# Kernel optimization log

Hardware: AMD Instinct MI355X
Metric: run time of the kernel (lower is better)

Reference implementation:

```python
import jax, jax.numpy as jnp
import numpy as np

B, S, D, H = 8, 2048, 1024, 16
HD = D // H  # head_dim = 64


def setup_inputs() -> dict:
    key = jax.random.key(0)
    ks = jax.random.split(key, 10)
    s = 0.02
    return {
        "x": jax.random.normal(ks[0], (B, S, D), jnp.float32),
        "mask": jnp.zeros((B, 1, S), jnp.float32),
        "Wq": jax.random.normal(ks[1], (D, D), jnp.float32) * s,
        "bq": jnp.zeros((D,), jnp.float32),
        "Wk": jax.random.normal(ks[2], (D, D), jnp.float32) * s,
        "bk": jnp.zeros((D,), jnp.float32),
        "Wv": jax.random.normal(ks[3], (D, D), jnp.float32) * s,
        "bv": jnp.zeros((D,), jnp.float32),
        "wa": jax.random.normal(ks[4], (HD, 1), jnp.float32) * s,
        "ba": jnp.zeros((1,), jnp.float32),
        "wb": jax.random.normal(ks[5], (HD, 1), jnp.float32) * s,
        "bb": jnp.zeros((1,), jnp.float32),
        "Wu": jax.random.normal(ks[6], (HD, HD), jnp.float32) * s,
        "bu": jnp.zeros((HD,), jnp.float32),
        "Wo": jax.random.normal(ks[7], (D, D), jnp.float32) * s,
        "bo": jnp.zeros((D,), jnp.float32),
        "gamma": jnp.ones((D,), jnp.float32),
        "beta_ln": jnp.zeros((D,), jnp.float32),
    }


def _split_heads(t):
    # [B,S,D] -> [B,H,S,HD]
    return t.reshape(B, S, H, HD).transpose(0, 2, 1, 3)


def reference(x, mask, Wq, bq, Wk, bk, Wv, bv, wa, ba, wb, bb, Wu, bu, Wo, bo, gamma, beta_ln):
    scale = 1.0 / jnp.sqrt(jnp.float32(HD))
    q = _split_heads(x @ Wq + bq)  # [B,H,S,HD]
    k = _split_heads(x @ Wk + bk)
    v = _split_heads(x @ Wv + bv)

    # additive attention over queries -> global query vector per head
    alphascore = (jnp.squeeze(q @ wa, -1) + ba[0]) * scale + mask  # [B,H,S]
    alphaw = jax.nn.softmax(alphascore, axis=-1)
    q_av = jnp.einsum('bhs,bhsd->bhd', alphaw, q)

    p = k * q_av[:, :, None, :]  # gated keys [B,H,S,HD]
    betascore = (jnp.squeeze(p @ wb, -1) + bb[0]) * scale + mask
    betaw = jax.nn.softmax(betascore, axis=-1)
    p_av = jnp.einsum('bhs,bhsd->bhd', betaw, p)

    u = v * p_av[:, :, None, :]  # gated values
    r = u @ Wu + bu  # [B,H,S,HD]
    newr = (r + q).transpose(0, 2, 1, 3).reshape(B, S, D)
    attn_out = newr @ Wo + bo

    h = x + attn_out
    mu = jnp.mean(h, axis=-1, keepdims=True)
    var = jnp.mean(jnp.square(h - mu), axis=-1, keepdims=True)
    return (h - mu) * jax.lax.rsqrt(var + 1e-6) * gamma + beta_ln
```

## Files before the change

### kernel.cpp

```cpp
#include <hip/hip_runtime.h>
#include <cstdint>

#define BB 8
#define SS 2048
#define DD 1024
#define HH 16
#define HDIM 64
#define MTOT (BB*SS)
#define QKVW 2048

typedef __attribute__((ext_vector_type(8))) __bf16 bf16x8;
typedef __attribute__((ext_vector_type(4))) float f32x4;

#define AS1(p) ((const __attribute__((address_space(1))) void*)(p))
#define AS3(p) ((__attribute__((address_space(3))) void*)(p))

__device__ __forceinline__ float bf2f(uint16_t u){
  return __uint_as_float(((uint32_t)u) << 16);
}
__device__ __forceinline__ uint16_t f2bf(float f){
  uint32_t u = __float_as_uint(f);
  return (uint16_t)((u + 0x7fffu + ((u >> 16) & 1u)) >> 16);
}

__global__ __launch_bounds__(256)
void k_prep(const float* __restrict__ x,
            const float* __restrict__ Wq, const float* __restrict__ Wk,
            const float* __restrict__ Wv, const float* __restrict__ Wo,
            const float* __restrict__ bq, const float* __restrict__ bv,
            uint16_t* __restrict__ xb, uint16_t* __restrict__ Wt,
            uint16_t* __restrict__ Wkt, uint16_t* __restrict__ WoT,
            float* __restrict__ bqv)
{
  __shared__ float t[32][33];
  const int blk = blockIdx.x, tid = threadIdx.x;
  if (blk < 2048){
    const int n4 = MTOT*DD/4;
    for (int i = blk*256 + tid; i < n4; i += 2048*256){
      float4 v = reinterpret_cast<const float4*>(x)[i];
      ushort4 o;
      o.x = f2bf(v.x); o.y = f2bf(v.y); o.z = f2bf(v.z); o.w = f2bf(v.w);
      reinterpret_cast<ushort4*>(xb)[i] = o;
    }
  } else if (blk < 6144){
    const int zb = blk - 2048;
    const int z = zb >> 10, rem = zb & 1023;
    const int by = rem >> 5, bx = rem & 31;
    const float* src = (z==0)?Wq:(z==1)?Wv:(z==2)?Wk:Wo;
    uint16_t* dst = (z==0)?Wt:(z==1)?(Wt + 1024*1024):(z==2)?Wkt:WoT;
    const int k0 = by*32, n0 = bx*32;
    const int tx = tid & 31, ty = tid >> 5;
    #pragma unroll
    for (int r = 0; r < 4; ++r)
      t[ty + r*8][tx] = src[(size_t)(k0 + ty + r*8)*1024 + n0 + tx];
    __syncthreads();
    #pragma unroll
    for (int r = 0; r < 4; ++r)
      dst[(size_t)(n0 + ty + r*8)*1024 + k0 + tx] = f2bf(t[tx][ty + r*8]);
  } else {
    const int i = (blk - 6144)*256 + tid;
    if (i < QKVW)
      bqv[i] = (i < 1024) ? bq[i] : bv[i-1024];
  }
}

#define BARRIER __builtin_amdgcn_s_barrier()

#define READA(BUF, MH) { \
  const uint16_t* _sl = lds + ((BUF)*4 + (MH))*8192; \
  _Pragma("unroll") \
  for (int f = 0; f < 4; ++f) \
    _Pragma("unroll") \
    for (int ks = 0; ks < 2; ++ks) \
      a[f][ks] = *(const bf16x8*)(_sl + (wm*64 + f*16 + l15)*64 + (((ks*4 + l4) ^ l7)<<3)); \
}

#define READB(BUF, NH, BV) { \
  const uint16_t* _sl = lds + ((BUF)*4 + 2 + (NH))*8192; \
  _Pragma("unroll") \
  for (int j = 0; j < 2; ++j) \
    _Pragma("unroll") \
    for (int ks = 0; ks < 2; ++ks) \
      BV[j][ks] = *(const bf16x8*)(_sl + (wn*32 + j*16 + l15)*64 + (((ks*4 + l4) ^ l7)<<3)); \
}

#define MMA(MH, NH, BV) { \
  __builtin_amdgcn_s_setprio(1); \
  _Pragma("unroll") \
  for (int ks = 0; ks < 2; ++ks) \
    _Pragma("unroll") \
    for (int f = 0; f < 4; ++f) \
      _Pragma("unroll") \
      for (int j = 0; j < 2; ++j) \
        acc[(MH)*4+f][(NH)*2+j] = __builtin_amdgcn_mfma_f32_16x16x32_bf16(a[f][ks], BV[j][ks], acc[(MH)*4+f][(NH)*2+j], 0, 0, 0); \
  __builtin_amdgcn_s_setprio(0); }

#define STAGEA(T, H) { \
  char* _d = (char*)lds + ((((T)&1)*4 + (H))*16384) + wave*1024; \
  _Pragma("unroll") \
  for (int l = 0; l < 2; ++l) \
    __builtin_amdgcn_global_load_lds(AS1(pA + (l*131072 + (H)*65536 + (T)*64)), AS3(_d + l*8192), 16, 0, 0); \
}

#define STAGEB(T, H) { \
  char* _d = (char*)lds + ((((T)&1)*4 + 2 + (H))*16384) + wave*1024; \
  _Pragma("unroll") \
  for (int l = 0; l < 2; ++l) \
    __builtin_amdgcn_global_load_lds(AS1(pB + (l*131072 + (H)*32768 + (T)*64)), AS3(_d + l*8192), 16, 0, 0); \
}

template<int EPI, int NB_T>
__global__ __launch_bounds__(512)
void k_gemm256(const uint16_t* __restrict__ A, const uint16_t* __restrict__ Bt,
               const float* __restrict__ bias, const uint16_t* __restrict__ resid16,
               uint16_t* __restrict__ Cout,
               const float* __restrict__ waP, const float* __restrict__ baP,
               const float* __restrict__ maskP,
               float* __restrict__ cpartA, float* __restrict__ dpartA)
{
  constexpr int N = NB_T * 256;
  __shared__ uint16_t lds[8 * 8192];
  const int tid = threadIdx.x;
  const int lane = tid & 63, wave = tid >> 6;
  const int wm = wave >> 2, wn = wave & 3;
  const int l15 = lane & 15, l4 = lane >> 4, l7 = lane & 7;

  const int nwg = gridDim.x, cpx = nwg >> 3, bid = blockIdx.x;
  const int wg = (bid & 7) * cpx + (bid >> 3);
  const int m0 = (wg / NB_T) << 8, n0 = (wg % NB_T) << 8;

  const int colbase = (((tid & 7) ^ ((tid >> 3) & 7)) << 3);
  const uint16_t* pA = A  + (size_t)(m0 + (tid >> 3)) * 1024 + colbase;
  const uint16_t* pB = Bt + (size_t)(n0 + ((tid >> 8) << 6) + ((tid >> 3) & 31)) * 1024 + colbase;

  f32x4 acc[8][4] = {};
  bf16x8 a[4][2], b0[2][2], b1[2][2];

  STAGEA(0,0); STAGEB(0,1); STAGEA(0,1); STAGEB(0,0);
  STAGEA(1,0); STAGEB(1,1); STAGEA(1,1);
  asm volatile("s_waitcnt vmcnt(6)" ::: "memory");
  BARRIER;

  #pragma unroll
  for (int I = 0; I < 7; ++I){
    const int e = 2*I;
    READA(0,0); READB(0,0,b0); STAGEB(e+1, 0);
    BARRIER; MMA(0,0,b0); BARRIER;
    READB(0,1,b1); STAGEA(e+2, 0);
    BARRIER; MMA(0,1,b1); BARRIER;
    READA(0,1); STAGEB(e+2, 1);
    BARRIER; MMA(1,1,b1); BARRIER;
    STAGEA(e+2, 1);
    asm volatile("s_waitcnt vmcnt(6)" ::: "memory");
    BARRIER; MMA(1,0,b0); BARRIER;
    READA(1,0); READB(1,0,b0); STAGEB(e+2, 0);
    BARRIER; MMA(0,0,b0); BARRIER;
    READB(1,1,b1); STAGEA(e+3, 0);
    BARRIER; MMA(0,1,b1); BARRIER;
    READA(1,1); STAGEB(e+3, 1);
    BARRIER; MMA(1,1,b1); BARRIER;
    STAGEA(e+3, 1);
    asm volatile("s_waitcnt vmcnt(6)" ::: "memory");
    BARRIER; MMA(1,0,b0); BARRIER;
  }

  {
    READA(0,0); READB(0,0,b0); STAGEB(15, 0);
    BARRIER; MMA(0,0,b0); BARRIER;
    READB(0,1,b1);
    BARRIER; MMA(0,1,b1); BARRIER;
    READA(0,1);
    BARRIER; MMA(1,1,b1); BARRIER;
    asm volatile("s_waitcnt vmcnt(0)" ::: "memory");
    BARRIER; MMA(1,0,b0); BARRIER;
    READA(1,0); READB(1,0,b0);
    BARRIER; MMA(0,0,b0); BARRIER;
    READB(1,1,b1);
    BARRIER; MMA(0,1,b1); BARRIER;
    READA(1,1);
    BARRIER; MMA(1,1,b1); BARRIER;
    MMA(1,0,b0);
  }

  #pragma unroll
  for (int mh = 0; mh < 2; ++mh)
  #pragma unroll
  for (int f = 0; f < 4; ++f)
  #pragma unroll
  for (int nh = 0; nh < 2; ++nh)
  #pragma unroll
  for (int j = 0; j < 2; ++j){
    const int gcol = n0 + wn*64 + nh*32 + j*16 + l15;
    const float bi = bias[gcol];
    const int rbase = m0 + wm*128 + mh*64 + f*16 + l4*4;
    #pragma unroll
    for (int rr = 0; rr < 4; ++rr){
      const size_t idx = (size_t)(rbase + rr)*N + gcol;
      float v = acc[mh*4+f][nh*2+j][rr] + bi;
      if (EPI == 1) v += bf2f(resid16[idx]);
      Cout[idx] = f2bf(v);
    }
  }

  if (EPI == 0 && n0 < 1024){
    const int hg = (n0 >> 6) + wn;
    const float bav = baP[0];
    float bcol[2][2], wv[2][2];
    #pragma unroll
    for (int nh = 0; nh < 2; ++nh)
    #pragma unroll
    for (int j = 0; j < 2; ++j){
      const int c = nh*32 + j*16 + l15;
      bcol[nh][j] = bias[n0 + wn*64 + c];
      wv[nh][j]   = waP[c];
    }
    float colacc[2][2] = {{0.f,0.f},{0.f,0.f}};
    float esum = 0.f;
    #pragma unroll
    for (int mh = 0; mh < 2; ++mh)
    #pragma unroll
    for (int f = 0; f < 4; ++f)
    #pragma unroll
    for (int rr = 0; rr < 4; ++rr){
      float qv[2][2];
      float p = 0.f;
      #pragma unroll
      for (int nh = 0; nh < 2; ++nh)
      #pragma unroll
      for (int j = 0; j < 2; ++j){
        qv[nh][j] = acc[mh*4+f][nh*2+j][rr] + bcol[nh][j];
        p += qv[nh][j] * wv[nh][j];
      }
      p += __shfl_xor(p, 1); p += __shfl_xor(p, 2);
      p += __shfl_xor(p, 4); p += __shfl_xor(p, 8);
      const int grow = m0 + wm*128 + mh*64 + f*16 + l4*4 + rr;
      const float E = __expf((p + bav)*0.125f + maskP[grow]);
      esum += E;
      #pragma unroll
      for (int nh = 0; nh < 2; ++nh)
      #pragma unroll
      for (int j = 0; j < 2; ++j)
        colacc[nh][j] += E * qv[nh][j];
    }
    const int rb = (m0 >> 7) + wm;
    #pragma unroll
    for (int nh = 0; nh < 2; ++nh)
    #pragma unroll
    for (int j = 0; j < 2; ++j){
      float v = colacc[nh][j];
      v += __shfl_xor(v, 16); v += __shfl_xor(v, 32);
      if (l4 == 0)
        cpartA[(size_t)rb*1024 + n0 + wn*64 + nh*32 + j*16 + l15] = v;
    }
    esum += __shfl_xor(esum, 16); esum += __shfl_xor(esum, 32);
    if (lane == 0) dpartA[rb*16 + hg] = esum;
  }
}

__global__ __launch_bounds__(256)
void k_mergeA(const float* __restrict__ cpartA, const float* __restrict__ dpartA,
              const float* __restrict__ wb,
              float* __restrict__ qavB, float* __restrict__ wvecB)
{
  __shared__ float dsum[16];
  const int blk = blockIdx.x, tid = threadIdx.x;
  const int b = blk >> 2, c = (blk & 3)*256 + tid;
  if (tid < 16){
    float d = 0.f;
    #pragma unroll
    for (int rb = 0; rb < 16; ++rb) d += dpartA[(b*16 + rb)*16 + tid];
    dsum[tid] = d;
  }
  __syncthreads();
  float s = 0.f;
  #pragma unroll
  for (int rb = 0; rb < 16; ++rb) s += cpartA[(size_t)(b*16 + rb)*1024 + c];
  const float qv = s / dsum[(c >> 6) & 15];
  qavB[b*1024 + c]  = qv;
  wvecB[b*1024 + c] = qv * wb[c & 63];
}

__global__ __launch_bounds__(256)
void k_foldB(const uint16_t* __restrict__ Wkt, const float* __restrict__ wvecB,
             const float* __restrict__ bk, const float* __restrict__ bbP,
             float* __restrict__ pBg, float* __restrict__ csB)
{
  __shared__ float wl[64];
  __shared__ float redc[64];
  const int bh = blockIdx.x, b = bh >> 4, h = bh & 15;
  const int tid = threadIdx.x;
  if (tid < 64) wl[tid] = wvecB[b*1024 + h*64 + tid];
  __syncthreads();
  const int k0 = tid*4;
  float a0 = 0.f, a1 = 0.f, a2 = 0.f, a3 = 0.f;
  for (int d = 0; d < 64; ++d){
    const float w = wl[d];
    const ushort4 r = *(const ushort4*)(Wkt + (size_t)(h*64 + d)*1024 + k0);
    a0 += bf2f(r.x)*w; a1 += bf2f(r.y)*w; a2 += bf2f(r.z)*w; a3 += bf2f(r.w)*w;
  }
  float* dst = pBg + (size_t)bh*1024 + k0;
  dst[0] = a0; dst[1] = a1; dst[2] = a2; dst[3] = a3;
  if (tid < 64) redc[tid] = bk[h*64 + tid] * wl[tid];
  __syncthreads();
  if (tid == 0){
    float s = 0.f;
    for (int i = 0; i < 64; ++i) s += redc[i];
    csB[bh] = s + bbP[0];
  }
}

__global__ __launch_bounds__(512)
void k_poolX(const uint16_t* __restrict__ xb, const float* __restrict__ pBg,
             const float* __restrict__ csB, const float* __restrict__ mask,
             float* __restrict__ xwp, float* __restrict__ dpartB)
{
  const int blk = blockIdx.x, tid = threadIdx.x;
  const int b = blk >> 5;
  const int h = tid >> 5, cs = tid & 31;
  const int col0 = cs*32;

  float pr[32];
  {
    const float4* p4 = (const float4*)(pBg + (size_t)(b*16 + h)*1024 + col0);
    #pragma unroll
    for (int i = 0; i < 8; ++i){
      const float4 t = p4[i];
      pr[4*i] = t.x; pr[4*i+1] = t.y; pr[4*i+2] = t.z; pr[4*i+3] = t.w;
    }
  }
  const float csh = csB[b*16 + h];
  float acc[32];
  #pragma unroll
  for (int i = 0; i < 32; ++i) acc[i] = 0.f;
  float esum = 0.f;

  const int row0 = blk*64;
  for (int r = 0; r < 64; ++r){
    const int row = row0 + r;
    const uint16_t* xr = xb + (size_t)row*1024 + col0;
    float xv[32];
    #pragma unroll
    for (int i = 0; i < 4; ++i){
      const bf16x8 v = *(const bf16x8*)(xr + i*8);
      #pragma unroll
      for (int e = 0; e < 8; ++e) xv[i*8+e] = (float)v[e];
    }
    float s = 0.f;
    #pragma unroll
    for (int i = 0; i < 32; ++i) s += xv[i]*pr[i];
    s += __shfl_xor(s, 1); s += __shfl_xor(s, 2); s += __shfl_xor(s, 4);
    s += __shfl_xor(s, 8); s += __shfl_xor(s, 16);
    const float E = __expf((s + csh)*0.125f + mask[row]);
    esum += E;
    #pragma unroll
    for (int i = 0; i < 32; ++i) acc[i] += E*xv[i];
  }
  float* dst = xwp + (size_t)(blk*16 + h)*1024 + col0;
  #pragma unroll
  for (int i = 0; i < 8; ++i)
    ((float4*)dst)[i] = (float4){acc[4*i], acc[4*i+1], acc[4*i+2], acc[4*i+3]};
  if (cs == 0) dpartB[blk*16 + h] = esum;
}

__global__ __launch_bounds__(512)
void k_finalB(const float* __restrict__ xwp, const float* __restrict__ dpartB,
              const float* __restrict__ qavB, const uint16_t* __restrict__ Wkt,
              const float* __restrict__ bk, const float* __restrict__ Wu,
              uint16_t* __restrict__ WuPT)
{
  __shared__ float xwl[1024];
  __shared__ float kvl[64];
  __shared__ float pavl[64];
  __shared__ float dsh;
  const int bh = blockIdx.x, b = bh >> 4, h = bh & 15;
  const int tid = threadIdx.x;
  #pragma unroll
  for (int i = 0; i < 2; ++i){
    const int idx = i*512 + tid;
    float s = 0.f;
    #pragma unroll
    for (int rc = 0; rc < 32; ++rc)
      s += xwp[((size_t)(b*32 + rc)*16 + h)*1024 + idx];
    xwl[idx] = s;
  }
  if (tid < 32){
    float d = dpartB[(b*32 + tid)*16 + h];
    d += __shfl_xor(d, 1); d += __shfl_xor(d, 2); d += __shfl_xor(d, 4);
    d += __shfl_xor(d, 8); d += __shfl_xor(d, 16);
    if (tid == 0) dsh = d;
  }
  __syncthreads();
  const int d = tid >> 3, q = tid & 7;
  const uint16_t* wrow = Wkt + (size_t)(h*64 + d)*1024 + q*128;
  const float* xwq = xwl + q*128;
  float s = 0.f;
  #pragma unroll
  for (int i = 0; i < 16; ++i){
    const bf16x8 v = *(const bf16x8*)(wrow + i*8);
    #pragma unroll
    for (int e = 0; e < 8; ++e) s += (float)v[e]*xwq[i*8+e];
  }
  s += __shfl_xor(s, 1); s += __shfl_xor(s, 2); s += __shfl_xor(s, 4);
  if (q == 0) kvl[d] = s;
  __syncthreads();
  if (tid < 64)
    pavl[tid] = qavB[b*1024 + h*64 + tid] * (kvl[tid]/dsh + bk[h*64 + tid]);
  __syncthreads();
  uint16_t* dst = WuPT + (size_t)bh*4096;
  for (int idx = tid; idx < 4096; idx += 512){
    const int i = idx & 63, jcol = idx >> 6;
    dst[idx] = f2bf(pavl[i]*Wu[i*64 + jcol]);
  }
}

__global__ __launch_bounds__(256)
void k_newr(const uint16_t* __restrict__ qkv, const uint16_t* __restrict__ WuPT,
            const float* __restrict__ bu, uint16_t* __restrict__ newr)
{
  const int bh = blockIdx.x >> 3, st = blockIdx.x & 7;
  const int b = bh >> 4, h = bh & 15;
  const int tid = threadIdx.x, wave = tid >> 6, lane = tid & 63;
  const int l15 = lane & 15, l4 = lane >> 4;
  const int s0 = st*256 + wave*64;
  const uint16_t* vb = qkv + 1024 + h*64;
  const uint16_t* wt = WuPT + (size_t)bh*4096;

  f32x4 acc[4][4] = {};
  #pragma unroll
  for (int ks = 0; ks < 2; ++ks){
    bf16x8 bfr[4];
    #pragma unroll
    for (int n = 0; n < 4; ++n)
      bfr[n] = *(const bf16x8*)(wt + (n*16 + l15)*64 + ks*32 + l4*8);
    #pragma unroll
    for (int m = 0; m < 4; ++m){
      const int s = s0 + m*16 + l15;
      bf16x8 af = *(const bf16x8*)(vb + (size_t)(b*SS + s)*QKVW + ks*32 + l4*8);
      #pragma unroll
      for (int n = 0; n < 4; ++n)
        acc[m][n] = __builtin_amdgcn_mfma_f32_16x16x32_bf16(af, bfr[n], acc[m][n], 0, 0, 0);
    }
  }
  #pragma unroll
  for (int n = 0; n < 4; ++n){
    const int j = n*16 + l15;
    const float bj = bu[j];
    #pragma unroll
    for (int m = 0; m < 4; ++m){
      #pragma unroll
      for (int r = 0; r < 4; ++r){
        const int s = s0 + m*16 + l4*4 + r;
        const size_t qidx = (size_t)(b*SS + s)*QKVW + h*64 + j;
        const float q = bf2f(qkv[qidx]);
        newr[(size_t)(b*SS + s)*DD + h*64 + j] = f2bf(acc[m][n][r] + bj + q);
      }
    }
  }
}

__global__ __launch_bounds__(256)
void k_ln(const uint16_t* __restrict__ h16, const float* __restrict__ gamma,
          const float* __restrict__ beta, float* __restrict__ out)
{
  __shared__ float r1[256], r2[256];
  const int row = blockIdx.x, tid = threadIdx.x;
  const ushort4 hv = ((const ushort4*)(h16 + (size_t)row*DD))[tid];
  float v0 = bf2f(hv.x), v1 = bf2f(hv.y), v2 = bf2f(hv.z), v3 = bf2f(hv.w);
  float s  = v0 + v1 + v2 + v3;
  float ss = v0*v0 + v1*v1 + v2*v2 + v3*v3;
  r1[tid] = s; r2[tid] = ss; __syncthreads();
  for (int off = 128; off > 0; off >>= 1){
    if (tid < off){ r1[tid] += r1[tid+off]; r2[tid] += r2[tid+off]; }
    __syncthreads();
  }
  const float mu  = r1[0]*(1.f/1024.f);
  const float var = r2[0]*(1.f/1024.f) - mu*mu;
  const float inv = rsqrtf(var + 1e-6f);
  const float4 g  = ((const float4*)gamma)[tid];
  const float4 be = ((const float4*)beta)[tid];
  float4 o;
  o.x = (v0-mu)*inv*g.x + be.x;
  o.y = (v1-mu)*inv*g.y + be.y;
  o.z = (v2-mu)*inv*g.z + be.z;
  o.w = (v3-mu)*inv*g.w + be.w;
  ((float4*)(out + (size_t)row*DD))[tid] = o;
}

extern "C" void kernel_launch(void* const* d_in, const int* in_sizes, int n_in,
                              void* d_out, int out_size, void* d_ws, size_t ws_size,
                              hipStream_t stream) {
  const float* x    = (const float*)d_in[0];
  const float* mask = (const float*)d_in[1];
  const float* Wq   = (const float*)d_in[2];
  const float* bq   = (const float*)d_in[3];
  const float* Wk   = (const float*)d_in[4];
  const float* bk   = (const float*)d_in[5];
  const float* Wv   = (const float*)d_in[6];
  const float* bv   = (const float*)d_in[7];
  const float* wa   = (const float*)d_in[8];
  const float* ba   = (const float*)d_in[9];
  const float* wb   = (const float*)d_in[10];
  const float* bb   = (const float*)d_in[11];
  const float* Wu   = (const float*)d_in[12];
  const float* bu   = (const float*)d_in[13];
  const float* Wo   = (const float*)d_in[14];
  const float* bo   = (const float*)d_in[15];
  const float* gamma= (const float*)d_in[16];
  const float* beta = (const float*)d_in[17];
  float* out = (float*)d_out;

  char* ws = (char*)d_ws;
  const size_t MB = 1ull << 20;
  uint16_t* xb    = (uint16_t*)(ws);
  uint16_t* Wt    = (uint16_t*)(ws + 32*MB);
  uint16_t* Wkt   = (uint16_t*)(ws + 36*MB);
  uint16_t* WoT   = (uint16_t*)(ws + 38*MB);
  float*    bqv   = (float*)   (ws + 40*MB);
  uint16_t* WuPT  = (uint16_t*)(ws + 41*MB);
  uint16_t* qkv   = (uint16_t*)(ws + 42*MB);
  uint16_t* hbuf16= (uint16_t*)(ws + 42*MB);
  float* cpartA = (float*)(ws + 110*MB);
  float* dpartA = (float*)(ws + 111*MB);
  float* qavB   = (float*)(ws + 112*MB);
  float* wvecB  = (float*)(ws + 113*MB);
  float* pBg    = (float*)(ws + 114*MB);
  float* csB    = (float*)(ws + 115*MB);
  float* dpartB = (float*)(ws + 116*MB);
  float* xwp    = (float*)(ws + 117*MB);
  uint16_t* newr= (uint16_t*)(ws + 138*MB);

  k_prep<<<6156, 256, 0, stream>>>(x, Wq, Wk, Wv, Wo, bq, bv, xb, Wt, Wkt, WoT, bqv);

  k_gemm256<0,8><<<(MTOT/256)*(QKVW/256), 512, 0, stream>>>(
      xb, Wt, bqv, nullptr, qkv, wa, ba, mask, cpartA, dpartA);

  k_mergeA<<<32, 256, 0, stream>>>(cpartA, dpartA, wb, qavB, wvecB);
  k_foldB<<<128, 256, 0, stream>>>(Wkt, wvecB, bk, bb, pBg, csB);
  k_poolX<<<256, 512, 0, stream>>>(xb, pBg, csB, mask, xwp, dpartB);
  k_finalB<<<128, 512, 0, stream>>>(xwp, dpartB, qavB, Wkt, bk, Wu, WuPT);

  k_newr<<<BB*HH*8, 256, 0, stream>>>(qkv, WuPT, bu, newr);
  k_gemm256<1,4><<<(MTOT/256)*(DD/256), 512, 0, stream>>>(
      newr, WoT, bo, xb, hbuf16, nullptr, nullptr, nullptr, nullptr, nullptr);
  k_ln<<<MTOT, 256, 0, stream>>>(hbuf16, gamma, beta, out);
}
```

Baseline: 235.6 us.

## Split beta pooling into MFMA score kernel and separate weighted x-sum kernel

```diff
diff --git a/kernel.cpp b/kernel.cpp
--- a/kernel.cpp
+++ b/kernel.cpp
@@ -283,7 +283,7 @@
 __global__ __launch_bounds__(256)
 void k_foldB(const uint16_t* __restrict__ Wkt, const float* __restrict__ wvecB,
              const float* __restrict__ bk, const float* __restrict__ bbP,
-             float* __restrict__ pBg, float* __restrict__ csB)
+             uint16_t* __restrict__ pBb, float* __restrict__ csB)
 {
   __shared__ float wl[64];
   __shared__ float redc[64];
@@ -298,8 +298,8 @@
     const ushort4 r = *(const ushort4*)(Wkt + (size_t)(h*64 + d)*1024 + k0);
     a0 += bf2f(r.x)*w; a1 += bf2f(r.y)*w; a2 += bf2f(r.z)*w; a3 += bf2f(r.w)*w;
   }
-  float* dst = pBg + (size_t)bh*1024 + k0;
-  dst[0] = a0; dst[1] = a1; dst[2] = a2; dst[3] = a3;
+  uint16_t* dst = pBb + (size_t)bh*1024 + k0;
+  dst[0] = f2bf(a0); dst[1] = f2bf(a1); dst[2] = f2bf(a2); dst[3] = f2bf(a3);
   if (tid < 64) redc[tid] = bk[h*64 + tid] * wl[tid];
   __syncthreads();
   if (tid == 0){
@@ -309,57 +309,77 @@
   }
 }
 
-__global__ __launch_bounds__(512)
-void k_poolX(const uint16_t* __restrict__ xb, const float* __restrict__ pBg,
-             const float* __restrict__ csB, const float* __restrict__ mask,
-             float* __restrict__ xwp, float* __restrict__ dpartB)
-{
+__global__ __launch_bounds__(256)
+void k_scoreM(const uint16_t* __restrict__ xb, const uint16_t* __restrict__ pBb,
+              const float* __restrict__ csB, const float* __restrict__ mask,
+              float* __restrict__ EB, float* __restrict__ dpartB)
+{
+  __shared__ float sred[4][16];
+  __shared__ float csl[16];
   const int blk = blockIdx.x, tid = threadIdx.x;
   const int b = blk >> 5;
-  const int h = tid >> 5, cs = tid & 31;
-  const int col0 = cs*32;
-
-  float pr[32];
-  {
-    const float4* p4 = (const float4*)(pBg + (size_t)(b*16 + h)*1024 + col0);
-    #pragma unroll
-    for (int i = 0; i < 8; ++i){
-      const float4 t = p4[i];
-      pr[4*i] = t.x; pr[4*i+1] = t.y; pr[4*i+2] = t.z; pr[4*i+3] = t.w;
-    }
-  }
-  const float csh = csB[b*16 + h];
-  float acc[32];
-  #pragma unroll
-  for (int i = 0; i < 32; ++i) acc[i] = 0.f;
-  float esum = 0.f;
-
+  const int wave = tid >> 6, lane = tid & 63;
+  const int l15 = lane & 15, l4 = lane >> 4;
+  if (tid < 16) csl[tid] = csB[b*16 + tid];
+  __syncthreads();
+  const int row0 = blk*64 + wave*16;
+  const uint16_t* pa = xb  + (size_t)(row0 + l15)*1024 + l4*8;
+  const uint16_t* pb = pBb + (size_t)(b*16 + l15)*1024 + l4*8;
+
+  f32x4 acc = {};
+  #pragma unroll
+  for (int kk = 0; kk < 32; ++kk){
+    const bf16x8 af = *(const bf16x8*)(pa + kk*32);
+    const bf16x8 bf = *(const bf16x8*)(pb + kk*32);
+    acc = __builtin_amdgcn_mfma_f32_16x16x32_bf16(af, bf, acc, 0, 0, 0);
+  }
+  float es = 0.f;
+  #pragma unroll
+  for (int r = 0; r < 4; ++r){
+    const int row = row0 + l4*4 + r;
+    const float E = __expf((acc[r] + csl[l15])*0.125f + mask[row]);
+    EB[(size_t)row*16 + l15] = E;
+    es += E;
+  }
+  es += __shfl_xor(es, 16); es += __shfl_xor(es, 32);
+  if (l4 == 0) sred[wave][l15] = es;
+  __syncthreads();
+  if (tid < 16)
+    dpartB[blk*16 + tid] = sred[0][tid] + sred[1][tid] + sred[2][tid] + sred[3][tid];
+}
+
+__global__ __launch_bounds__(256)
+void k_xsumV(const uint16_t* __restrict__ xb, const float* __restrict__ EB,
+             float* __restrict__ xwp)
+{
+  const int blk = blockIdx.x, tid = threadIdx.x;
   const int row0 = blk*64;
+  const int c0 = tid*4;
+  float acc[16][4];
+  #pragma unroll
+  for (int h = 0; h < 16; ++h){
+    #pragma unroll
+    for (int c = 0; c < 4; ++c) acc[h][c] = 0.f;
+  }
   for (int r = 0; r < 64; ++r){
     const int row = row0 + r;
-    const uint16_t* xr = xb + (size_t)row*1024 + col0;
-    float xv[32];
-    #pragma unroll
-    for (int i = 0; i < 4; ++i){
-      const bf16x8 v = *(const bf16x8*)(xr + i*8);
-      #pragma unroll
-      for (int e = 0; e < 8; ++e) xv[i*8+e] = (float)v[e];
-    }
-    float s = 0.f;
-    #pragma unroll
-    for (int i = 0; i < 32; ++i) s += xv[i]*pr[i];
-    s += __shfl_xor(s, 1); s += __shfl_xor(s, 2); s += __shfl_xor(s, 4);
-    s += __shfl_xor(s, 8); s += __shfl_xor(s, 16);
-    const float E = __expf((s + csh)*0.125f + mask[row]);
-    esum += E;
-    #pragma unroll
-    for (int i = 0; i < 32; ++i) acc[i] += E*xv[i];
-  }
-  float* dst = xwp + (size_t)(blk*16 + h)*1024 + col0;
-  #pragma unroll
-  for (int i = 0; i < 8; ++i)
-    ((float4*)dst)[i] = (float4){acc[4*i], acc[4*i+1], acc[4*i+2], acc[4*i+3]};
-  if (cs == 0) dpartB[blk*16 + h] = esum;
+    const ushort4 xv4 = *(const ushort4*)(xb + (size_t)row*1024 + c0);
+    const float x0 = bf2f(xv4.x), x1 = bf2f(xv4.y), x2 = bf2f(xv4.z), x3 = bf2f(xv4.w);
+    const float4* e4 = (const float4*)(EB + (size_t)row*16);
+    const float4 e0 = e4[0], e1 = e4[1], e2 = e4[2], e3 = e4[3];
+    #define ACCH(hh, ee) { acc[hh][0] += x0*(ee); acc[hh][1] += x1*(ee); \
+                           acc[hh][2] += x2*(ee); acc[hh][3] += x3*(ee); }
+    ACCH(0,  e0.x) ACCH(1,  e0.y) ACCH(2,  e0.z) ACCH(3,  e0.w)
+    ACCH(4,  e1.x) ACCH(5,  e1.y) ACCH(6,  e1.z) ACCH(7,  e1.w)
+    ACCH(8,  e2.x) ACCH(9,  e2.y) ACCH(10, e2.z) ACCH(11, e2.w)
+    ACCH(12, e3.x) ACCH(13, e3.y) ACCH(14, e3.z) ACCH(15, e3.w)
+    #undef ACCH
+  }
+  float* dst = xwp + (size_t)blk*16*1024;
+  #pragma unroll
+  for (int h = 0; h < 16; ++h)
+    *(float4*)(dst + h*1024 + c0) =
+        (float4){acc[h][0], acc[h][1], acc[h][2], acc[h][3]};
 }
 
 __global__ __launch_bounds__(512)
@@ -523,10 +543,11 @@
   float* dpartA = (float*)(ws + 111*MB);
   float* qavB   = (float*)(ws + 112*MB);
   float* wvecB  = (float*)(ws + 113*MB);
-  float* pBg    = (float*)(ws + 114*MB);
+  uint16_t* pBb = (uint16_t*)(ws + 114*MB);
   float* csB    = (float*)(ws + 115*MB);
-  float* dpartB = (float*)(ws + 116*MB);
-  float* xwp    = (float*)(ws + 117*MB);
+  float* EB     = (float*)(ws + 116*MB);
+  float* dpartB = (float*)(ws + 118*MB);
+  float* xwp    = (float*)(ws + 119*MB);
   uint16_t* newr= (uint16_t*)(ws + 138*MB);
 
   k_prep<<<6156, 256, 0, stream>>>(x, Wq, Wk, Wv, Wo, bq, bv, xb, Wt, Wkt, WoT, bqv);
@@ -535,8 +556,9 @@
       xb, Wt, bqv, nullptr, qkv, wa, ba, mask, cpartA, dpartA);
 
   k_mergeA<<<32, 256, 0, stream>>>(cpartA, dpartA, wb, qavB, wvecB);
-  k_foldB<<<128, 256, 0, stream>>>(Wkt, wvecB, bk, bb, pBg, csB);
-  k_poolX<<<256, 512, 0, stream>>>(xb, pBg, csB, mask, xwp, dpartB);
+  k_foldB<<<128, 256, 0, stream>>>(Wkt, wvecB, bk, bb, pBb, csB);
+  k_scoreM<<<256, 256, 0, stream>>>(xb, pBb, csB, mask, EB, dpartB);
+  k_xsumV<<<256, 256, 0, stream>>>(xb, EB, xwp);
   k_finalB<<<128, 512, 0, stream>>>(xwp, dpartB, qavB, Wkt, bk, Wu, WuPT);
 
   k_newr<<<BB*HH*8, 256, 0, stream>>>(qkv, WuPT, bu, newr);
```

New measurement: 221.2 us. 6.1% less time.
